# Kernel optimization log

Measured on AMD Instinct MI355X. Metric: run time of the kernel, lower is better.

Reference implementation:

```python
import jax, jax.numpy as jnp
import numpy as np

EXPERT_NUM = 8
SEQ_LEN = 2048
FREQ_LEN = SEQ_LEN // 2 + 1
B, C = 32, 512


def setup_inputs() -> dict:
    key = jax.random.key(0)
    k1, k2, k3 = jax.random.split(key, 3)
    x = jax.random.normal(k1, (B, C, SEQ_LEN), dtype=jnp.float32)
    band_boundaries = jax.random.uniform(k2, (EXPERT_NUM - 1,), dtype=jnp.float32)
    gate_w = jax.random.normal(k3, (EXPERT_NUM, FREQ_LEN), dtype=jnp.float32) / np.sqrt(FREQ_LEN)
    gate_b = jnp.zeros((EXPERT_NUM,), dtype=jnp.float32)
    return {"x": x, "band_boundaries": band_boundaries, "gate_w": gate_w, "gate_b": gate_b}


def reference(x, band_boundaries, gate_w, gate_b):
    # x: [B, C, L].  Normalize across channels per (batch, time) position.
    xp = jnp.transpose(x, (0, 2, 1))                       # [B, L, C]
    x_mean = jnp.mean(xp, axis=2, keepdims=True)           # [B, L, 1]
    xc = xp - x_mean
    x_var = jnp.var(xc, axis=2, keepdims=True, ddof=1) + 1e-5  # unbiased, as torch.var
    xn = xc / jnp.sqrt(x_var)
    x_norm = jnp.transpose(xn, (0, 2, 1))                  # [B, C, L]

    freq_x = jnp.fft.rfft(x_norm, axis=-1)                 # [B, C, F] complex
    F = FREQ_LEN

    # Learnable band boundaries -> integer bin boundaries per expert.
    b = jnp.sort(jax.nn.sigmoid(band_boundaries))
    b = jnp.concatenate([jnp.zeros((1,), b.dtype), b, jnp.ones((1,), b.dtype)])
    idx = (b * F).astype(jnp.int32)
    idx = idx.at[-1].set(F)                                # [E+1]

    # Per-frequency-bin expert membership: [E, F] 0/1 mask.
    f = jnp.arange(F)
    member = ((f[None, :] >= idx[:-1, None]) & (f[None, :] < idx[1:, None])).astype(x.dtype)

    # Gating over mean spectral magnitude.
    gating_input = jnp.abs(freq_x).mean(axis=1)            # [B, F]
    gating_scores = jax.nn.softmax(gating_input @ gate_w.T + gate_b, axis=-1)  # [B, E]

    # Fused: per-bin gate weight = sum_e g[b,e] * member[e,f] (no E copies of freq_x).
    w = gating_scores @ member                             # [B, F]
    combined_freq = freq_x * w[:, None, :].astype(freq_x.dtype)

    combined = jnp.fft.irfft(combined_freq, n=SEQ_LEN, axis=-1)  # [B, C, L]

    # De-normalize.
    cp = jnp.transpose(combined, (0, 2, 1))                # [B, L, C]
    out = cp * jnp.sqrt(x_var) + x_mean
    return jnp.transpose(out, (0, 2, 1))                   # [B, C, L]
```

## Files before the change

### kernel.cpp

```cpp
#include <hip/hip_runtime.h>
#include <math.h>

#define NB 32
#define NC 512
#define NF 1025

#define WS_MEAN 0
#define WS_SSTD 65536
#define WS_RSTD 131072
#define WS_GACC 196608
#define WS_WGT  229408
#define WS_PART 262208
#define WS_END_SPLIT (262208 + 262144)
#define WS_SPEC WS_END_SPLIT
#define WS_SPEC_FLOATS (NB * NC * 2048)
#define WS_END_CACHE (WS_SPEC + WS_SPEC_FLOATS)
#define WS_GPART WS_END_CACHE
#define WS_GPART_FLOATS (NB * 64 * NF)
#define WS_END_GPART (WS_GPART + WS_GPART_FLOATS)

#define PIDX(a) ((a) + ((a) >> 4))

__device__ __forceinline__ void lds_barrier() {
  __builtin_amdgcn_sched_barrier(0);
  asm volatile("s_waitcnt lgkmcnt(0)" ::: "memory");
  __builtin_amdgcn_s_barrier();
  __builtin_amdgcn_sched_barrier(0);
}

__device__ __forceinline__ void stage4_body(const float* __restrict__ sr,
                                            const float* __restrict__ si,
                                            float* __restrict__ dr,
                                            float* __restrict__ di,
                                            const int ls, const float w1c, const float w1s,
                                            const bool fwd) {
  const int t = threadIdx.x;
  const int s = 1 << ls;
  const int q = t & (s - 1);
  const int p = t >> ls;
  const float ar = sr[PIDX(t)],       ai = si[PIDX(t)];
  const float br = sr[PIDX(t + 256)], bi = si[PIDX(t + 256)];
  const float cr = sr[PIDX(t + 512)], ci = si[PIDX(t + 512)];
  const float er = sr[PIDX(t + 768)], ei = si[PIDX(t + 768)];
  const float apcr = ar + cr, apci = ai + ci;
  const float amcr = ar - cr, amci = ai - ci;
  const float bpdr = br + er, bpdi = bi + ei;
  const float bmdr = br - er, bmdi = bi - ei;
  const float w2r = w1c * w1c - w1s * w1s, w2i = 2.0f * w1c * w1s;
  const float w3r = w2r * w1c - w2i * w1s, w3i = w2r * w1s + w2i * w1c;
  float u1r, u1i, u3r, u3i;
  if (fwd) {
    u1r = amcr + bmdi; u1i = amci - bmdr;
    u3r = amcr - bmdi; u3i = amci + bmdr;
  } else {
    u1r = amcr - bmdi; u1i = amci + bmdr;
    u3r = amcr + bmdi; u3i = amci - bmdr;
  }
  const float x0r = apcr + bpdr, x0i = apci + bpdi;
  const float v2r = apcr - bpdr, v2i = apci - bpdi;
  const float x1r = w1c * u1r - w1s * u1i, x1i = w1c * u1i + w1s * u1r;
  const float x2r = w2r * v2r - w2i * v2i, x2i = w2r * v2i + w2i * v2r;
  const float x3r = w3r * u3r - w3i * u3i, x3i = w3r * u3i + w3i * u3r;
  const int base = q + ((p << 2) << ls);
  dr[PIDX(base)] = x0r;             di[PIDX(base)] = x0i;
  dr[PIDX(base + s)] = x1r;         di[PIDX(base + s)] = x1i;
  dr[PIDX(base + 2 * s)] = x2r;     di[PIDX(base + 2 * s)] = x2i;
  dr[PIDX(base + 3 * s)] = x3r;     di[PIDX(base + 3 * s)] = x3i;
}

__device__ __forceinline__ void stage4(const float* __restrict__ sr,
                                       const float* __restrict__ si,
                                       float* __restrict__ dr,
                                       float* __restrict__ di,
                                       const int ls, const float w1c, const float w1s,
                                       const bool fwd) {
  lds_barrier();
  stage4_body(sr, si, dr, di, ls, w1c, w1s, fwd);
}

__device__ __forceinline__ void stage0_reg(const float2 z0, const float2 z1,
                                           const float2 z2, const float2 z3,
                                           float* __restrict__ dr, float* __restrict__ di,
                                           const float w1c, const float w1s,
                                           const bool fwd) {
  const int t = threadIdx.x;
  const float apcr = z0.x + z2.x, apci = z0.y + z2.y;
  const float amcr = z0.x - z2.x, amci = z0.y - z2.y;
  const float bpdr = z1.x + z3.x, bpdi = z1.y + z3.y;
  const float bmdr = z1.x - z3.x, bmdi = z1.y - z3.y;
  const float w2r = w1c * w1c - w1s * w1s, w2i = 2.0f * w1c * w1s;
  const float w3r = w2r * w1c - w2i * w1s, w3i = w2r * w1s + w2i * w1c;
  float u1r, u1i, u3r, u3i;
  if (fwd) {
    u1r = amcr + bmdi; u1i = amci - bmdr;
    u3r = amcr - bmdi; u3i = amci + bmdr;
  } else {
    u1r = amcr - bmdi; u1i = amci + bmdr;
    u3r = amcr + bmdi; u3i = amci - bmdr;
  }
  const float x0r = apcr + bpdr, x0i = apci + bpdi;
  const float v2r = apcr - bpdr, v2i = apci - bpdi;
  const float x1r = w1c * u1r - w1s * u1i, x1i = w1c * u1i + w1s * u1r;
  const float x2r = w2r * v2r - w2i * v2i, x2i = w2r * v2i + w2i * v2r;
  const float x3r = w3r * u3r - w3i * u3i, x3i = w3r * u3i + w3i * u3r;
  const int base = t << 2;
  dr[PIDX(base)] = x0r;         di[PIDX(base)] = x0i;
  dr[PIDX(base + 1)] = x1r;     di[PIDX(base + 1)] = x1i;
  dr[PIDX(base + 2)] = x2r;     di[PIDX(base + 2)] = x2i;
  dr[PIDX(base + 3)] = x3r;     di[PIDX(base + 3)] = x3i;
}

__device__ __forceinline__ void stage_nt_body(const float* __restrict__ sr,
                                              const float* __restrict__ si,
                                              float2& o0, float2& o1, float2& o2, float2& o3,
                                              const bool fwd) {
  const int t = threadIdx.x;
  const float ar = sr[PIDX(t)],       ai = si[PIDX(t)];
  const float br = sr[PIDX(t + 256)], bi = si[PIDX(t + 256)];
  const float cr = sr[PIDX(t + 512)], ci = si[PIDX(t + 512)];
  const float er = sr[PIDX(t + 768)], ei = si[PIDX(t + 768)];
  const float apcr = ar + cr, apci = ai + ci;
  const float amcr = ar - cr, amci = ai - ci;
  const float bpdr = br + er, bpdi = bi + ei;
  const float bmdr = br - er, bmdi = bi - ei;
  float u1r, u1i, u3r, u3i;
  if (fwd) {
    u1r = amcr + bmdi; u1i = amci - bmdr;
    u3r = amcr - bmdi; u3i = amci + bmdr;
  } else {
    u1r = amcr - bmdi; u1i = amci + bmdr;
    u3r = amcr + bmdi; u3i = amci - bmdr;
  }
  o0.x = apcr + bpdr;  o0.y = apci + bpdi;
  o1.x = u1r;          o1.y = u1i;
  o2.x = apcr - bpdr;  o2.y = apci - bpdi;
  o3.x = u3r;          o3.y = u3i;
}

__device__ __forceinline__ void stage_nt_reg(const float* __restrict__ sr,
                                             const float* __restrict__ si,
                                             float2& o0, float2& o1, float2& o2, float2& o3,
                                             const bool fwd) {
  lds_barrier();
  stage_nt_body(sr, si, o0, o1, o2, o3, fwd);
}

__device__ __forceinline__ void fft_twiddles(int t, float& c0, float& s0,
                                             float& c1, float& s1,
                                             float& c2, float& s2,
                                             float& c3, float& s3) {
  __sincosf(-0.00613592315f * (float)t, &s0, &c0);
  __sincosf(-0.02454369261f * (float)(t >> 2), &s1, &c1);
  __sincosf(-0.09817477042f * (float)(t >> 4), &s2, &c2);
  __sincosf(-0.39269908170f * (float)(t >> 6), &s3, &c3);
}

__global__ __launch_bounds__(256) void kmoments(const float* __restrict__ x,
                                                float* __restrict__ ws) {
  const int b = blockIdx.x >> 3;
  const int l = ((blockIdx.x & 7) << 8) + threadIdx.x;
  const float* px = x + (size_t)b * (NC * 2048) + l;
  float sum = 0.f, sq = 0.f;
#pragma unroll 16
  for (int c = 0; c < NC; ++c) {
    float v = px[(size_t)c * 2048];
    sum += v;
    sq = fmaf(v, v, sq);
  }
  float mean = sum * (1.0f / 512.0f);
  float var = fmaf(-512.0f * mean, mean, sq) * (1.0f / 511.0f) + 1e-5f;
  float ss = sqrtf(var);
  int o = (b << 11) + l;
  ws[WS_MEAN + o] = mean;
  ws[WS_SSTD + o] = ss;
  ws[WS_RSTD + o] = 1.0f / ss;
}

__global__ __launch_bounds__(256) void kmoments_part(const float* __restrict__ x,
                                                     float* __restrict__ ws) {
  const int b = blockIdx.x >> 3;
  const int l = ((blockIdx.x & 7) << 8) + threadIdx.x;
  const int half = blockIdx.y;
  const float* px = x + (size_t)b * (NC * 2048) + (size_t)(half * 256) * 2048 + l;
  float sum = 0.f, sq = 0.f;
#pragma unroll 16
  for (int c = 0; c < 256; ++c) {
    float v = px[(size_t)c * 2048];
    sum += v;
    sq = fmaf(v, v, sq);
  }
  int o = (b << 11) + l;
  float2* part = (float2*)(ws + WS_PART) + (half << 16) + o;
  float2 pv; pv.x = sum; pv.y = sq;
  *part = pv;
}

__global__ __launch_bounds__(256) void kmoments_fin(float* __restrict__ ws) {
  const int o = blockIdx.x * 256 + threadIdx.x;
  const float2* part = (const float2*)(ws + WS_PART);
  float2 p0 = part[o];
  float2 p1 = part[(1 << 16) + o];
  float sum = p0.x + p1.x, sq = p0.y + p1.y;
  float mean = sum * (1.0f / 512.0f);
  float var = fmaf(-512.0f * mean, mean, sq) * (1.0f / 511.0f) + 1e-5f;
  float ss = sqrtf(var);
  ws[WS_MEAN + o] = mean;
  ws[WS_SSTD + o] = ss;
  ws[WS_RSTD + o] = 1.0f / ss;
}

__global__ __launch_bounds__(256) void kspec(const float* __restrict__ x,
                                             float* __restrict__ ws,
                                             float2* __restrict__ zout,
                                             float* __restrict__ gpart) {
  __shared__ float Ar[1088], Ai[1088], Br[1088], Bi[1088];
  const int tid = threadIdx.x;
  const int b = blockIdx.x >> 6;
  const int c0 = (blockIdx.x & 63) << 3;
  const float2* mean2 = (const float2*)(ws + WS_MEAN) + ((size_t)b << 10);
  const float2* rstd2 = (const float2*)(ws + WS_RSTD) + ((size_t)b << 10);
  float2 mv[4], rv[4];
#pragma unroll
  for (int j = 0; j < 4; ++j) {
    mv[j] = mean2[tid + (j << 8)];
    rv[j] = rstd2[tid + (j << 8)];
  }
  float w1s, w1c, w2s, w2c;
  __sincosf(-0.00306796158f * (float)tid, &w1s, &w1c);
  __sincosf(-0.00306796158f * (float)(tid + 256), &w2s, &w2c);
  float c0t, s0t, c1t, s1t, c2t, s2t, c3t, s3t;
  fft_twiddles(tid, c0t, s0t, c1t, s1t, c2t, s2t, c3t, s3t);
  float acc0 = 0.f, acc1 = 0.f, acc2 = 0.f, acc3 = 0.f, acc4 = 0.f;
  const float2* xrow = (const float2*)x + ((size_t)(b * NC + c0) << 10);
  float2 v[4];
#pragma unroll
  for (int j = 0; j < 4; ++j) v[j] = xrow[tid + (j << 8)];
  for (int r = 0; r < 8; ++r) {
    float2 zz[4];
#pragma unroll
    for (int j = 0; j < 4; ++j) {
      zz[j].x = (v[j].x - mv[j].x) * rv[j].x;
      zz[j].y = (v[j].y - mv[j].y) * rv[j].y;
    }
    if (r < 7) {
      const float2* nx = xrow + ((size_t)(r + 1) << 10);
#pragma unroll
      for (int j = 0; j < 4; ++j) v[j] = nx[tid + (j << 8)];
    }
    lds_barrier();
    stage0_reg(zz[0], zz[1], zz[2], zz[3], Br, Bi, c0t, s0t, true);
    stage4(Br, Bi, Ar, Ai, 2, c1t, s1t, true);
    stage4(Ar, Ai, Br, Bi, 4, c2t, s2t, true);
    stage4(Br, Bi, Ar, Ai, 6, c3t, s3t, true);
    float2 o0, o1, o2, o3;
    stage_nt_reg(Ar, Ai, o0, o1, o2, o3, true);
    Br[PIDX(tid)] = o0.x;        Bi[PIDX(tid)] = o0.y;
    Br[PIDX(tid + 256)] = o1.x;  Bi[PIDX(tid + 256)] = o1.y;
    Br[PIDX(tid + 512)] = o2.x;  Bi[PIDX(tid + 512)] = o2.y;
    Br[PIDX(tid + 768)] = o3.x;  Bi[PIDX(tid + 768)] = o3.y;
    lds_barrier();
    if (zout) {
      float2* zrow = zout + ((size_t)(b * NC + c0 + r) << 10);
      zrow[tid] = o0;
      zrow[tid + 256] = o1;
      zrow[tid + 512] = o2;
      zrow[tid + 768] = o3;
    }
    if (tid == 0) {
      float zr = Br[PIDX(0)], zi = Bi[PIDX(0)];
      acc0 += fabsf(zr + zi);
      acc1 += fabsf(zr - zi);
      float mr = Br[PIDX(512)], mi = Bi[PIDX(512)];
      acc4 += sqrtf(mr * mr + mi * mi);
    } else {
      const int k = tid;
      float zkr = Br[PIDX(k)], zki = Bi[PIDX(k)];
      float zmr = Br[PIDX(1024 - k)], zmi = Bi[PIDX(1024 - k)];
      float Ar_ = 0.5f * (zkr + zmr), Ai_ = 0.5f * (zki - zmi);
      float Br_ = 0.5f * (zki + zmi), Bi_ = -0.5f * (zkr - zmr);
      float WBr = Br_ * w1c - Bi_ * w1s, WBi = Br_ * w1s + Bi_ * w1c;
      float Xr = Ar_ + WBr, Xi = Ai_ + WBi;
      float Yr = Ar_ - WBr, Yi = Ai_ - WBi;
      acc0 += sqrtf(Xr * Xr + Xi * Xi);
      acc1 += sqrtf(Yr * Yr + Yi * Yi);
    }
    {
      const int k = tid + 256;
      float zkr = Br[PIDX(k)], zki = Bi[PIDX(k)];
      float zmr = Br[PIDX(1024 - k)], zmi = Bi[PIDX(1024 - k)];
      float Ar_ = 0.5f * (zkr + zmr), Ai_ = 0.5f * (zki - zmi);
      float Br_ = 0.5f * (zki + zmi), Bi_ = -0.5f * (zkr - zmr);
      float WBr = Br_ * w2c - Bi_ * w2s, WBi = Br_ * w2s + Bi_ * w2c;
      float Xr = Ar_ + WBr, Xi = Ai_ + WBi;
      float Yr = Ar_ - WBr, Yi = Ai_ - WBi;
      acc2 += sqrtf(Xr * Xr + Xi * Xi);
      acc3 += sqrtf(Yr * Yr + Yi * Yi);
    }
  }
  if (gpart) {
    float* prow = gpart + (size_t)blockIdx.x * NF;
    prow[tid] = acc0;
    prow[1024 - tid] = acc1;
    prow[tid + 256] = acc2;
    prow[768 - tid] = acc3;
    if (tid == 0) prow[512] = acc4;
  } else {
    float* g = ws + WS_GACC + b * NF;
    atomicAdd(g + tid, acc0);
    atomicAdd(g + 1024 - tid, acc1);
    atomicAdd(g + tid + 256, acc2);
    atomicAdd(g + 768 - tid, acc3);
    if (tid == 0) atomicAdd(g + 512, acc4);
  }
}

__global__ __launch_bounds__(256) void kgate(float* __restrict__ ws,
                                             const float* __restrict__ gw,
                                             const float* __restrict__ gb,
                                             const float* __restrict__ bb,
                                             const float* __restrict__ gpart) {
  const float* gacc = ws + WS_GACC;
  float* wgt = ws + WS_WGT;
  const int b = blockIdx.x;
  const int tid = threadIdx.x;
  __shared__ float red[256];
  __shared__ float sc[8];
  __shared__ int sidx[9];
  float acc[8];
#pragma unroll
  for (int e = 0; e < 8; ++e) acc[e] = 0.f;
  for (int f = tid; f < NF; f += 256) {
    float g;
    if (gpart) {
      const float* gp = gpart + (size_t)b * 64 * NF + f;
      g = 0.f;
#pragma unroll 8
      for (int j = 0; j < 64; ++j) g += gp[j * NF];
    } else {
      g = gacc[b * NF + f];
    }
    g *= (1.0f / 512.0f);
#pragma unroll
    for (int e = 0; e < 8; ++e) acc[e] = fmaf(g, gw[e * NF + f], acc[e]);
  }
#pragma unroll
  for (int e = 0; e < 8; ++e) {
    __syncthreads();
    red[tid] = acc[e];
    __syncthreads();
    for (int s2 = 128; s2 > 0; s2 >>= 1) {
      if (tid < s2) red[tid] += red[tid + s2];
      __syncthreads();
    }
    if (tid == 0) sc[e] = red[0] + gb[e];
  }
  __syncthreads();
  if (tid == 0) {
    float mx = sc[0];
    for (int e = 1; e < 8; ++e) mx = fmaxf(mx, sc[e]);
    float sum = 0.f;
    float ex[8];
    for (int e = 0; e < 8; ++e) { ex[e] = expf(sc[e] - mx); sum += ex[e]; }
    for (int e = 0; e < 8; ++e) sc[e] = ex[e] / sum;
    float sv[7];
    for (int i2 = 0; i2 < 7; ++i2) sv[i2] = 1.0f / (1.0f + expf(-bb[i2]));
    for (int i2 = 1; i2 < 7; ++i2) {
      float key = sv[i2];
      int j2 = i2 - 1;
      while (j2 >= 0 && sv[j2] > key) { sv[j2 + 1] = sv[j2]; --j2; }
      sv[j2 + 1] = key;
    }
    sidx[0] = 0;
    for (int i2 = 0; i2 < 7; ++i2) sidx[i2 + 1] = (int)(sv[i2] * 1025.0f);
    sidx[8] = 1025;
  }
  __syncthreads();
  for (int f = tid; f < NF; f += 256) {
    float wv = 0.f;
#pragma unroll
    for (int e = 0; e < 8; ++e)
      if (f >= sidx[e] && f < sidx[e + 1]) wv += sc[e];
    wgt[b * NF + f] = wv;
  }
}

__device__ __forceinline__ void combine_pair(float* __restrict__ zr_, float* __restrict__ zi_,
                                             int k, float wc, float ws_, float wk, float wmk) {
  const int ik = PIDX(k), im = PIDX(1024 - k);
  float zkr = zr_[ik], zki = zi_[ik];
  float zmr = zr_[im], zmi = zi_[im];
  float Ar_ = 0.5f * (zkr + zmr), Ai_ = 0.5f * (zki - zmi);
  float Br2 = 0.5f * (zki + zmi), Bi2 = -0.5f * (zkr - zmr);
  float WBr = Br2 * wc - Bi2 * ws_, WBi = Br2 * ws_ + Bi2 * wc;
  float Xr = Ar_ + WBr, Xi = Ai_ + WBi;
  float Xcr = Ar_ - WBr, Xci = Ai_ - WBi;
  float XpR = wk * Xr, XpI = wk * Xi;
  float XcpR = wmk * Xcr, XcpI = wmk * Xci;
  float Apr = 0.5f * (XpR + XcpR), Api = 0.5f * (XpI + XcpI);
  float Er = 0.5f * (XpR - XcpR), Ei = 0.5f * (XpI - XcpI);
  float Bpr = Er * wc + Ei * ws_;
  float Bpi = Ei * wc - Er * ws_;
  zr_[ik] = Apr - Bpi;  zi_[ik] = Api + Bpr;
  zr_[im] = Apr + Bpi;  zi_[im] = Bpr - Api;
}

__device__ __forceinline__ void combine_all(float* __restrict__ Br_, float* __restrict__ Bi_,
                                            const int tid,
                                            const float w1c, const float w1s,
                                            const float w2c, const float w2s,
                                            const float wk1, const float wm1,
                                            const float wk2, const float wm2,
                                            const float wmid) {
  if (tid == 0) {
    float zr = Br_[PIDX(0)], zi = Bi_[PIDX(0)];
    float X0 = (zr + zi) * wk1;
    float XM = (zr - zi) * wm1;
    Br_[PIDX(0)] = 0.5f * (X0 + XM);
    Bi_[PIDX(0)] = 0.5f * (X0 - XM);
    Br_[PIDX(512)] *= wmid;
    Bi_[PIDX(512)] *= wmid;
  } else {
    combine_pair(Br_, Bi_, tid, w1c, w1s, wk1, wm1);
  }
  combine_pair(Br_, Bi_, tid + 256, w2c, w2s, wk2, wm2);
}

__global__ __launch_bounds__(256) void kapply(const float* __restrict__ x,
                                              float* __restrict__ out,
                                              const float* __restrict__ ws) {
  __shared__ float Ar[1088], Ai[1088], Br[1088], Bi[1088];
  const int tid = threadIdx.x;
  const int b = blockIdx.x >> 9;
  const float2* mean2 = (const float2*)(ws + WS_MEAN) + ((size_t)b << 10);
  const float2* sstd2 = (const float2*)(ws + WS_SSTD) + ((size_t)b << 10);
  const float2* rstd2 = (const float2*)(ws + WS_RSTD) + ((size_t)b << 10);
  const float2* x2 = (const float2*)x + ((size_t)blockIdx.x << 10);
  const float* wrow = ws + WS_WGT + b * NF;
  float wk1 = wrow[tid];
  float wm1 = wrow[1024 - tid];
  float wk2 = wrow[tid + 256];
  float wm2 = wrow[768 - tid];
  float wmid = wrow[512];
  float w1s, w1c, w2s, w2c;
  __sincosf(-0.00306796158f * (float)tid, &w1s, &w1c);
  __sincosf(-0.00306796158f * (float)(tid + 256), &w2s, &w2c);
  float c0t, s0t, c1t, s1t, c2t, s2t, c3t, s3t;
  fft_twiddles(tid, c0t, s0t, c1t, s1t, c2t, s2t, c3t, s3t);
  float2 mv[4], rv[4], ssv[4];
#pragma unroll
  for (int j = 0; j < 4; ++j) {
    mv[j] = mean2[tid + (j << 8)];
    rv[j] = rstd2[tid + (j << 8)];
    ssv[j] = sstd2[tid + (j << 8)];
  }
  float2 zz[4];
#pragma unroll
  for (int j = 0; j < 4; ++j) {
    float2 v = x2[tid + (j << 8)];
    zz[j].x = (v.x - mv[j].x) * rv[j].x;
    zz[j].y = (v.y - mv[j].y) * rv[j].y;
  }
  stage0_reg(zz[0], zz[1], zz[2], zz[3], Br, Bi, c0t, s0t, true);
  stage4(Br, Bi, Ar, Ai, 2, c1t, s1t, true);
  stage4(Ar, Ai, Br, Bi, 4, c2t, s2t, true);
  stage4(Br, Bi, Ar, Ai, 6, c3t, s3t, true);
  float2 f0, f1, f2, f3;
  stage_nt_reg(Ar, Ai, f0, f1, f2, f3, true);
  Br[PIDX(tid)] = f0.x;        Bi[PIDX(tid)] = f0.y;
  Br[PIDX(tid + 256)] = f1.x;  Bi[PIDX(tid + 256)] = f1.y;
  Br[PIDX(tid + 512)] = f2.x;  Bi[PIDX(tid + 512)] = f2.y;
  Br[PIDX(tid + 768)] = f3.x;  Bi[PIDX(tid + 768)] = f3.y;
  lds_barrier();
  combine_all(Br, Bi, tid, w1c, w1s, w2c, w2s, wk1, wm1, wk2, wm2, wmid);
  stage4(Br, Bi, Ar, Ai, 0, c0t, -s0t, false);
  stage4(Ar, Ai, Br, Bi, 2, c1t, -s1t, false);
  stage4(Br, Bi, Ar, Ai, 4, c2t, -s2t, false);
  stage4(Ar, Ai, Br, Bi, 6, c3t, -s3t, false);
  float2 o0, o1, o2, o3;
  stage_nt_reg(Br, Bi, o0, o1, o2, o3, false);
  const float inv = 1.0f / 1024.0f;
  float2* out2 = (float2*)out + ((size_t)blockIdx.x << 10);
  float2 oo;
  oo.x = fmaf(o0.x * inv, ssv[0].x, mv[0].x);
  oo.y = fmaf(o0.y * inv, ssv[0].y, mv[0].y);
  out2[tid] = oo;
  oo.x = fmaf(o1.x * inv, ssv[1].x, mv[1].x);
  oo.y = fmaf(o1.y * inv, ssv[1].y, mv[1].y);
  out2[tid + 256] = oo;
  oo.x = fmaf(o2.x * inv, ssv[2].x, mv[2].x);
  oo.y = fmaf(o2.y * inv, ssv[2].y, mv[2].y);
  out2[tid + 512] = oo;
  oo.x = fmaf(o3.x * inv, ssv[3].x, mv[3].x);
  oo.y = fmaf(o3.y * inv, ssv[3].y, mv[3].y);
  out2[tid + 768] = oo;
}

__global__ __launch_bounds__(256) void kapply_z(const float2* __restrict__ z,
                                                float* __restrict__ out,
                                                const float* __restrict__ ws) {
  __shared__ float Ar[1088], Ai[1088], Br[1088], Bi[1088];
  const int tid = threadIdx.x;
  const int b = blockIdx.x >> 9;
  const float2* mean2 = (const float2*)(ws + WS_MEAN) + ((size_t)b << 10);
  const float2* sstd2 = (const float2*)(ws + WS_SSTD) + ((size_t)b << 10);
  const float* wrow = ws + WS_WGT + b * NF;
  float wk1 = wrow[tid];
  float wm1 = wrow[1024 - tid];
  float wk2 = wrow[tid + 256];
  float wm2 = wrow[768 - tid];
  float wmid = wrow[512];
  float w1s, w1c, w2s, w2c;
  __sincosf(-0.00306796158f * (float)tid, &w1s, &w1c);
  __sincosf(-0.00306796158f * (float)(tid + 256), &w2s, &w2c);
  float c0t, s0t, c1t, s1t, c2t, s2t, c3t, s3t;
  fft_twiddles(tid, c0t, s0t, c1t, s1t, c2t, s2t, c3t, s3t);
  const float2* zrow = z + ((size_t)blockIdx.x << 10);
  float2 mv[4], ssv[4];
#pragma unroll
  for (int j = 0; j < 4; ++j) {
    mv[j] = mean2[tid + (j << 8)];
    ssv[j] = sstd2[tid + (j << 8)];
  }
#pragma unroll
  for (int j = 0; j < 4; ++j) {
    const int n = tid + (j << 8);
    float2 v = zrow[n];
    Br[PIDX(n)] = v.x;
    Bi[PIDX(n)] = v.y;
  }
  lds_barrier();
  combine_all(Br, Bi, tid, w1c, w1s, w2c, w2s, wk1, wm1, wk2, wm2, wmid);
  stage4(Br, Bi, Ar, Ai, 0, c0t, -s0t, false);
  stage4(Ar, Ai, Br, Bi, 2, c1t, -s1t, false);
  stage4(Br, Bi, Ar, Ai, 4, c2t, -s2t, false);
  stage4(Ar, Ai, Br, Bi, 6, c3t, -s3t, false);
  float2 o0, o1, o2, o3;
  stage_nt_reg(Br, Bi, o0, o1, o2, o3, false);
  const float inv = 1.0f / 1024.0f;
  float2* out2 = (float2*)out + ((size_t)blockIdx.x << 10);
  float2 oo;
  oo.x = fmaf(o0.x * inv, ssv[0].x, mv[0].x);
  oo.y = fmaf(o0.y * inv, ssv[0].y, mv[0].y);
  out2[tid] = oo;
  oo.x = fmaf(o1.x * inv, ssv[1].x, mv[1].x);
  oo.y = fmaf(o1.y * inv, ssv[1].y, mv[1].y);
  out2[tid + 256] = oo;
  oo.x = fmaf(o2.x * inv, ssv[2].x, mv[2].x);
  oo.y = fmaf(o2.y * inv, ssv[2].y, mv[2].y);
  out2[tid + 512] = oo;
  oo.x = fmaf(o3.x * inv, ssv[3].x, mv[3].x);
  oo.y = fmaf(o3.y * inv, ssv[3].y, mv[3].y);
  out2[tid + 768] = oo;
}

extern "C" void kernel_launch(void* const* d_in, const int* in_sizes, int n_in,
                              void* d_out, int out_size, void* d_ws, size_t ws_size,
                              hipStream_t stream) {
  const float* x = (const float*)d_in[0];
  const float* bb = (const float*)d_in[1];
  const float* gw = (const float*)d_in[2];
  const float* gb = (const float*)d_in[3];
  float* ws = (float*)d_ws;
  float* out = (float*)d_out;

  const bool split = ws_size >= (size_t)WS_END_SPLIT * sizeof(float);
  const bool cache = ws_size >= (size_t)WS_END_CACHE * sizeof(float);
  const bool part = ws_size >= (size_t)WS_END_GPART * sizeof(float);

  if (!part) {
    hipMemsetAsync((char*)d_ws + WS_GACC * sizeof(float), 0, (NB * NF) * sizeof(float), stream);
  }
  if (split) {
    kmoments_part<<<dim3(NB * 8, 2), dim3(256), 0, stream>>>(x, ws);
    kmoments_fin<<<dim3(256), dim3(256), 0, stream>>>(ws);
  } else {
    kmoments<<<dim3(NB * 8), dim3(256), 0, stream>>>(x, ws);
  }
  kspec<<<dim3(NB * 64), dim3(256), 0, stream>>>(x, ws,
      cache ? (float2*)(ws + WS_SPEC) : nullptr,
      part ? (ws + WS_GPART) : nullptr);
  kgate<<<dim3(NB), dim3(256), 0, stream>>>(ws, gw, gb, bb,
      part ? (ws + WS_GPART) : nullptr);
  if (cache) {
    kapply_z<<<dim3(NB * NC), dim3(256), 0, stream>>>((const float2*)(ws + WS_SPEC), out, ws);
  } else {
    kapply<<<dim3(NB * NC), dim3(256), 0, stream>>>(x, out, ws);
  }
}
```

Baseline: 352.2 us.

## Recompute forward FFT in apply kernel instead of caching spectrum in workspace

Removes the path where kspec writes the full complex spectrum to workspace and kapply_z reads it back. The apply kernel now always recomputes the forward FFT from x. This trades a large global write plus read for extra FFT arithmetic. kgate now stores only the 8 softmax scores and band boundaries per batch, and each apply thread builds its per-bin weights in registers, which drops the per-bin weight array and its global reads.

```diff
diff --git a/kernel.cpp b/kernel.cpp
--- a/kernel.cpp
+++ b/kernel.cpp
@@ -12,10 +12,7 @@
 #define WS_WGT  229408
 #define WS_PART 262208
 #define WS_END_SPLIT (262208 + 262144)
-#define WS_SPEC WS_END_SPLIT
-#define WS_SPEC_FLOATS (NB * NC * 2048)
-#define WS_END_CACHE (WS_SPEC + WS_SPEC_FLOATS)
-#define WS_GPART WS_END_CACHE
+#define WS_GPART WS_END_SPLIT
 #define WS_GPART_FLOATS (NB * 64 * NF)
 #define WS_END_GPART (WS_GPART + WS_GPART_FLOATS)
 
@@ -211,7 +208,6 @@
 
 __global__ __launch_bounds__(256) void kspec(const float* __restrict__ x,
                                              float* __restrict__ ws,
-                                             float2* __restrict__ zout,
                                              float* __restrict__ gpart) {
   __shared__ float Ar[1088], Ai[1088], Br[1088], Bi[1088];
   const int tid = threadIdx.x;
@@ -259,13 +255,6 @@
     Br[PIDX(tid + 512)] = o2.x;  Bi[PIDX(tid + 512)] = o2.y;
     Br[PIDX(tid + 768)] = o3.x;  Bi[PIDX(tid + 768)] = o3.y;
     lds_barrier();
-    if (zout) {
-      float2* zrow = zout + ((size_t)(b * NC + c0 + r) << 10);
-      zrow[tid] = o0;
-      zrow[tid + 256] = o1;
-      zrow[tid + 512] = o2;
-      zrow[tid + 768] = o3;
-    }
     if (tid == 0) {
       float zr = Br[PIDX(0)], zi = Bi[PIDX(0)];
       acc0 += fabsf(zr + zi);
@@ -320,12 +309,9 @@
                                              const float* __restrict__ bb,
                                              const float* __restrict__ gpart) {
   const float* gacc = ws + WS_GACC;
-  float* wgt = ws + WS_WGT;
   const int b = blockIdx.x;
   const int tid = threadIdx.x;
   __shared__ float red[256];
-  __shared__ float sc[8];
-  __shared__ int sidx[9];
   float acc[8];
 #pragma unroll
   for (int e = 0; e < 8; ++e) acc[e] = 0.f;
@@ -343,6 +329,7 @@
 #pragma unroll
     for (int e = 0; e < 8; ++e) acc[e] = fmaf(g, gw[e * NF + f], acc[e]);
   }
+  float sc[8];
 #pragma unroll
   for (int e = 0; e < 8; ++e) {
     __syncthreads();
@@ -354,7 +341,6 @@
     }
     if (tid == 0) sc[e] = red[0] + gb[e];
   }
-  __syncthreads();
   if (tid == 0) {
     float mx = sc[0];
     for (int e = 1; e < 8; ++e) mx = fmaxf(mx, sc[e]);
@@ -370,17 +356,11 @@
       while (j2 >= 0 && sv[j2] > key) { sv[j2 + 1] = sv[j2]; --j2; }
       sv[j2 + 1] = key;
     }
-    sidx[0] = 0;
-    for (int i2 = 0; i2 < 7; ++i2) sidx[i2 + 1] = (int)(sv[i2] * 1025.0f);
-    sidx[8] = 1025;
-  }
-  __syncthreads();
-  for (int f = tid; f < NF; f += 256) {
-    float wv = 0.f;
-#pragma unroll
-    for (int e = 0; e < 8; ++e)
-      if (f >= sidx[e] && f < sidx[e + 1]) wv += sc[e];
-    wgt[b * NF + f] = wv;
+    float* srow = ws + WS_WGT + (b << 5);
+    for (int e = 0; e < 8; ++e) srow[e] = sc[e];
+    srow[8] = 0.0f;
+    for (int i2 = 0; i2 < 7; ++i2) srow[9 + i2] = (float)((int)(sv[i2] * 1025.0f));
+    srow[16] = 1025.0f;
   }
 }
 
@@ -435,12 +415,24 @@
   const float2* sstd2 = (const float2*)(ws + WS_SSTD) + ((size_t)b << 10);
   const float2* rstd2 = (const float2*)(ws + WS_RSTD) + ((size_t)b << 10);
   const float2* x2 = (const float2*)x + ((size_t)blockIdx.x << 10);
-  const float* wrow = ws + WS_WGT + b * NF;
-  float wk1 = wrow[tid];
-  float wm1 = wrow[1024 - tid];
-  float wk2 = wrow[tid + 256];
-  float wm2 = wrow[768 - tid];
-  float wmid = wrow[512];
+  const float* srow = ws + WS_WGT + (b << 5);
+  float scv[8], siv[9];
+#pragma unroll
+  for (int e = 0; e < 8; ++e) scv[e] = srow[e];
+#pragma unroll
+  for (int e = 0; e < 9; ++e) siv[e] = srow[8 + e];
+#define BANDW(ff, dst) { float wv = 0.f; \
+    _Pragma("unroll") \
+    for (int e = 0; e < 8; ++e) \
+      wv += ((ff) >= siv[e] && (ff) < siv[e + 1]) ? scv[e] : 0.f; \
+    dst = wv; }
+  float wk1, wm1, wk2, wm2, wmid;
+  BANDW((float)tid, wk1);
+  BANDW((float)(1024 - tid), wm1);
+  BANDW((float)(tid + 256), wk2);
+  BANDW((float)(768 - tid), wm2);
+  BANDW(512.0f, wmid);
+#undef BANDW
   float w1s, w1c, w2s, w2c;
   __sincosf(-0.00306796158f * (float)tid, &w1s, &w1c);
   __sincosf(-0.00306796158f * (float)(tid + 256), &w2s, &w2c);
@@ -495,64 +487,6 @@
   out2[tid + 768] = oo;
 }
 
-__global__ __launch_bounds__(256) void kapply_z(const float2* __restrict__ z,
-                                                float* __restrict__ out,
-                                                const float* __restrict__ ws) {
-  __shared__ float Ar[1088], Ai[1088], Br[1088], Bi[1088];
-  const int tid = threadIdx.x;
-  const int b = blockIdx.x >> 9;
-  const float2* mean2 = (const float2*)(ws + WS_MEAN) + ((size_t)b << 10);
-  const float2* sstd2 = (const float2*)(ws + WS_SSTD) + ((size_t)b << 10);
-  const float* wrow = ws + WS_WGT + b * NF;
-  float wk1 = wrow[tid];
-  float wm1 = wrow[1024 - tid];
-  float wk2 = wrow[tid + 256];
-  float wm2 = wrow[768 - tid];
-  float wmid = wrow[512];
-  float w1s, w1c, w2s, w2c;
-  __sincosf(-0.00306796158f * (float)tid, &w1s, &w1c);
-  __sincosf(-0.00306796158f * (float)(tid + 256), &w2s, &w2c);
-  float c0t, s0t, c1t, s1t, c2t, s2t, c3t, s3t;
-  fft_twiddles(tid, c0t, s0t, c1t, s1t, c2t, s2t, c3t, s3t);
-  const float2* zrow = z + ((size_t)blockIdx.x << 10);
-  float2 mv[4], ssv[4];
-#pragma unroll
-  for (int j = 0; j < 4; ++j) {
-    mv[j] = mean2[tid + (j << 8)];
-    ssv[j] = sstd2[tid + (j << 8)];
-  }
-#pragma unroll
-  for (int j = 0; j < 4; ++j) {
-    const int n = tid + (j << 8);
-    float2 v = zrow[n];
-    Br[PIDX(n)] = v.x;
-    Bi[PIDX(n)] = v.y;
-  }
-  lds_barrier();
-  combine_all(Br, Bi, tid, w1c, w1s, w2c, w2s, wk1, wm1, wk2, wm2, wmid);
-  stage4(Br, Bi, Ar, Ai, 0, c0t, -s0t, false);
-  stage4(Ar, Ai, Br, Bi, 2, c1t, -s1t, false);
-  stage4(Br, Bi, Ar, Ai, 4, c2t, -s2t, false);
-  stage4(Ar, Ai, Br, Bi, 6, c3t, -s3t, false);
-  float2 o0, o1, o2, o3;
-  stage_nt_reg(Br, Bi, o0, o1, o2, o3, false);
-  const float inv = 1.0f / 1024.0f;
-  float2* out2 = (float2*)out + ((size_t)blockIdx.x << 10);
-  float2 oo;
-  oo.x = fmaf(o0.x * inv, ssv[0].x, mv[0].x);
-  oo.y = fmaf(o0.y * inv, ssv[0].y, mv[0].y);
-  out2[tid] = oo;
-  oo.x = fmaf(o1.x * inv, ssv[1].x, mv[1].x);
-  oo.y = fmaf(o1.y * inv, ssv[1].y, mv[1].y);
-  out2[tid + 256] = oo;
-  oo.x = fmaf(o2.x * inv, ssv[2].x, mv[2].x);
-  oo.y = fmaf(o2.y * inv, ssv[2].y, mv[2].y);
-  out2[tid + 512] = oo;
-  oo.x = fmaf(o3.x * inv, ssv[3].x, mv[3].x);
-  oo.y = fmaf(o3.y * inv, ssv[3].y, mv[3].y);
-  out2[tid + 768] = oo;
-}
-
 extern "C" void kernel_launch(void* const* d_in, const int* in_sizes, int n_in,
                               void* d_out, int out_size, void* d_ws, size_t ws_size,
                               hipStream_t stream) {
@@ -564,7 +498,6 @@
   float* out = (float*)d_out;
 
   const bool split = ws_size >= (size_t)WS_END_SPLIT * sizeof(float);
-  const bool cache = ws_size >= (size_t)WS_END_CACHE * sizeof(float);
   const bool part = ws_size >= (size_t)WS_END_GPART * sizeof(float);
 
   if (!part) {
@@ -577,13 +510,8 @@
     kmoments<<<dim3(NB * 8), dim3(256), 0, stream>>>(x, ws);
   }
   kspec<<<dim3(NB * 64), dim3(256), 0, stream>>>(x, ws,
-      cache ? (float2*)(ws + WS_SPEC) : nullptr,
       part ? (ws + WS_GPART) : nullptr);
   kgate<<<dim3(NB), dim3(256), 0, stream>>>(ws, gw, gb, bb,
       part ? (ws + WS_GPART) : nullptr);
-  if (cache) {
-    kapply_z<<<dim3(NB * NC), dim3(256), 0, stream>>>((const float2*)(ws + WS_SPEC), out, ws);
-  } else {
-    kapply<<<dim3(NB * NC), dim3(256), 0, stream>>>(x, out, ws);
-  }
-}
+  kapply<<<dim3(NB * NC), dim3(256), 0, stream>>>(x, out, ws);
+}
```

Result: slower. 377.5 us (+7.2%).
